# Kernel tuning notes

Measured on AMD Instinct MI355X. Metric: run time of the kernel, lower is better.

The kernel has to match this reference:

```python
import jax, jax.numpy as jnp
import numpy as np

B, L, M = 8192, 64, 64
LOCAL_DIM, MAX_UP, MAX_DN = 4, 64, 64


def setup_inputs() -> dict:
    key = jax.random.key(0)
    k1, k2 = jax.random.split(key)
    # occupation indices per site: 0=empty, 1=up, 2=down, 3=both
    indices = jax.random.randint(k1, (B, L), 0, LOCAL_DIM, dtype=jnp.int64)
    # learned GPS parameter tensor (local_dim, M, L, max_up+1, max_dn+1);
    # centered near 1 so the product over L sites stays numerically stable
    epsilon = 1.0 + 0.05 * jax.random.normal(
        k2, (LOCAL_DIM, M, L, MAX_UP + 1, MAX_DN + 1), dtype=jnp.float32)
    return {"indices": indices, "epsilon": epsilon}


def reference(indices, epsilon):
    b, l = indices.shape
    # cumulative particle counts of sites strictly before site i
    n_up = jnp.pad(jnp.cumsum(indices[:, :-1] & 1, axis=-1), ((0, 0), (1, 0)))
    n_dn = jnp.pad(jnp.cumsum((indices[:, :-1] & 2) // 2, axis=-1), ((0, 0), (1, 0)))
    site_ar = jnp.arange(l)[None, :]  # (1, L)
    # multi-axis gather: site_vals[b, i, m] = epsilon[idx[b,i], m, i, n_up[b,i], n_dn[b,i]]
    site_vals = epsilon[indices, :, site_ar, n_up, n_dn]  # (B, L, M)
    # product over sites, sum over GPS rank M
    log_psi = jnp.sum(jnp.prod(site_vals, axis=1), axis=-1)  # (B,)
    return log_psi
```

## Files before the change

kernel.cpp:

```cpp
#include <hip/hip_runtime.h>
#include <hip/hip_fp16.h>


#define TAB_HALF_BYTES ((size_t)89440 * 256 * 2)

__global__ __launch_bounds__(256) void seggps_init(int* __restrict__ ranges) {
  int t = threadIdx.x;
  if (t < 64) {
    ranges[t] = 64;
    ranges[64 + t] = -1;
    ranges[128 + t] = 64;
    ranges[192 + t] = -1;
  }
}

__global__ __launch_bounds__(256) void seggps_ranges(
    const int* __restrict__ indices, int* __restrict__ ranges) {
  __shared__ int s_umin[64], s_umax[64], s_nmin[64], s_nmax[64];
  int t = threadIdx.x;
  if (t < 64) { s_umin[t] = 64; s_umax[t] = -1; s_nmin[t] = 64; s_nmax[t] = -1; }
  __syncthreads();
  int wave = t >> 6, lane = t & 63;
  for (int i = 0; i < 16; ++i) {
    int b = blockIdx.x * 64 + wave * 16 + i;
    int v = indices[b * 64 + lane];
    int up = v & 1, dn = (v >> 1) & 1;
#pragma unroll
    for (int s = 1; s < 64; s <<= 1) {
      int au = __shfl_up(up, s, 64);
      int ad = __shfl_up(dn, s, 64);
      if (lane >= s) { up += au; dn += ad; }
    }
    int eu = up - (v & 1);
    int ed = dn - ((v >> 1) & 1);
    atomicMin(&s_umin[lane], eu); atomicMax(&s_umax[lane], eu);
    atomicMin(&s_nmin[lane], ed); atomicMax(&s_nmax[lane], ed);
  }
  __syncthreads();
  if (t < 64) {
    atomicMin(&ranges[t], s_umin[t]);
    atomicMax(&ranges[64 + t], s_umax[t]);
    atomicMin(&ranges[128 + t], s_nmin[t]);
    atomicMax(&ranges[192 + t], s_nmax[t]);
  }
}

__global__ __launch_bounds__(256) void seggps_transpose(
    const float* __restrict__ eps, __half* __restrict__ tab,
    const int* __restrict__ ranges) {
  int bid = blockIdx.x;
  int d = bid / 2080;
  int t = bid % 2080;
  int l = (int)((sqrtf(8.0f * (float)t + 1.0f) - 1.0f) * 0.5f);
  while ((l + 1) * (l + 2) / 2 <= t) ++l;
  while (l * (l + 1) / 2 > t) --l;
  int u = t - l * (l + 1) / 2;

  int umin = ranges[l], umax = ranges[64 + l];
  if (u < umin || u > umax) return;
  int nmin = ranges[128 + l], nmax = ranges[192 + l];

  int lane = threadIdx.x & 63;
  int wave = threadIdx.x >> 6;

  __shared__ float tile[64][65];

  const float* src = eps + ((size_t)(d * 64) * 64 + l) * 4225 + u * 65;
  if (lane >= nmin && lane <= nmax) {
#pragma unroll 4
    for (int m = wave; m < 64; m += 4) {
      tile[m][lane] = __builtin_nontemporal_load(&src[(size_t)m * 270400 + lane]);
    }
  }
  __syncthreads();

  int Pl = l * (l + 1) * (2 * l + 1) / 6;
  __half* dst = tab + (size_t)(Pl + u * (l + 1)) * 256 + d * 64 + lane;
  for (int n = nmin + wave; n <= nmax; n += 4) {
    dst[n * 256] = __float2half(tile[lane][n]);
  }
}

__global__ __launch_bounds__(256, 4) void seggps_main(
    const int* __restrict__ indices, const __half* __restrict__ tab,
    float* __restrict__ out) {
  int wave = threadIdx.x >> 6;
  int lane = threadIdx.x & 63;
  int g = lane >> 4;
  int Lm = lane & 15;
  int b0 = (blockIdx.x * 4 + wave) * 4;

  int ipk = indices[(b0 + 0) * 64 + lane]
          | (indices[(b0 + 1) * 64 + lane] << 2)
          | (indices[(b0 + 2) * 64 + lane] << 4)
          | (indices[(b0 + 3) * 64 + lane] << 6);

  float p0 = 1.f, p1 = 1.f, p2 = 1.f, p3 = 1.f;
  int up = 0, dn = 0;
  int Pl = 0;
  int mbase = Lm * 4;
#pragma unroll 16
  for (int l = 0; l < 64; ++l) {
    int s = __shfl(ipk, l, 64);
    int v = (s >> (2 * g)) & 3;
    int o = (Pl + up * (l + 1) + dn) * 256 + v * 64 + mbase;
    ushort4 q = *reinterpret_cast<const ushort4*>(tab + o);
    p0 *= __half2float(__ushort_as_half(q.x));
    p1 *= __half2float(__ushort_as_half(q.y));
    p2 *= __half2float(__ushort_as_half(q.z));
    p3 *= __half2float(__ushort_as_half(q.w));
    up += v & 1;
    dn += (v >> 1) & 1;
    Pl += (l + 1) * (l + 1);
  }
  float r = (p0 + p1) + (p2 + p3);
#pragma unroll
  for (int s = 8; s; s >>= 1) r += __shfl_down(r, s, 16);
  if (Lm == 0) out[b0 + g] = r;
}

__global__ __launch_bounds__(256) void seggps_direct(
    const int* __restrict__ indices, const float* __restrict__ eps,
    float* __restrict__ out) {
  int wave = threadIdx.x >> 6;
  int lane = threadIdx.x & 63;
  int b = blockIdx.x * 4 + wave;

  int myidx = indices[b * 64 + lane];

  float p0 = 1.f, p1 = 1.f, p2 = 1.f, p3 = 1.f;
  int up = 0, dn = 0;
#pragma unroll 8
  for (int l = 0; l < 64; ++l) {
    int v = __shfl(myidx, l, 64);
    size_t off = ((size_t)((v * 64 + lane) * 64 + l)) * 4225 + up * 65 + dn;
    float e = eps[off];
    if ((l & 3) == 0)      p0 *= e;
    else if ((l & 3) == 1) p1 *= e;
    else if ((l & 3) == 2) p2 *= e;
    else                   p3 *= e;
    up += v & 1;
    dn += (v >> 1) & 1;
  }
  float p = (p0 * p1) * (p2 * p3);
#pragma unroll
  for (int s = 32; s; s >>= 1) p += __shfl_down(p, s, 64);
  if (lane == 0) out[b] = p;
}

extern "C" void kernel_launch(void* const* d_in, const int* in_sizes, int n_in,
                              void* d_out, int out_size, void* d_ws, size_t ws_size,
                              hipStream_t stream) {
  const int* indices = (const int*)d_in[0];
  const float* eps   = (const float*)d_in[1];
  float* out = (float*)d_out;

  if (ws_size >= TAB_HALF_BYTES + 1024) {
    __half* tab = (__half*)d_ws;
    int* ranges = (int*)((char*)d_ws + TAB_HALF_BYTES);
    hipLaunchKernelGGL(seggps_init, dim3(1), dim3(256), 0, stream, ranges);
    hipLaunchKernelGGL(seggps_ranges, dim3(128), dim3(256), 0, stream,
                       indices, ranges);
    hipLaunchKernelGGL(seggps_transpose, dim3(4 * 2080), dim3(256), 0, stream,
                       eps, tab, ranges);
    hipLaunchKernelGGL(seggps_main, dim3(8192 / 16), dim3(256), 0, stream,
                       indices, tab, out);
  } else {
    hipLaunchKernelGGL(seggps_direct, dim3(8192 / 4), dim3(256), 0, stream,
                       indices, eps, out);
  }
}
```

Before: 341.8 us.

## Fuse four-kernel pipeline into one cooperative kernel with grid syncs

Replaces the init, ranges, transpose and main launches with a single cooperative kernel of 512 blocks that separates the phases with grid-wide syncs. The goal is to remove per-launch overhead and the tail gaps between kernels. The prefix count is now computed with ballot plus popcount instead of a shuffle scan, and the nontemporal load hint is dropped. In exchange, the transpose phase now runs on only 512 persistent blocks looping over 8320 items instead of 8320 independent blocks, which can cut memory-level parallelism. The grid barriers also add their own cost.

Result: slower. 500.5 us (+46.4%).

```diff
diff --git a/kernel.cpp b/kernel.cpp
--- a/kernel.cpp
+++ b/kernel.cpp
@@ -1,8 +1,120 @@
 #include <hip/hip_runtime.h>
 #include <hip/hip_fp16.h>
+#include <hip/hip_cooperative_groups.h>
+
+namespace cg = cooperative_groups;
 
 
 #define TAB_HALF_BYTES ((size_t)89440 * 256 * 2)
+
+__global__ __launch_bounds__(256, 2) void seggps_fused(
+    const int* __restrict__ indices, const float* __restrict__ eps,
+    __half* __restrict__ tab, int* __restrict__ ranges,
+    float* __restrict__ out) {
+  cg::grid_group grid = cg::this_grid();
+  __shared__ float tile[64][65];
+  __shared__ int s_umin[64], s_umax[64], s_nmin[64], s_nmax[64];
+
+  int t = threadIdx.x;
+  int wave = t >> 6, lane = t & 63;
+  int blk = blockIdx.x;
+
+  if (blk == 0 && t < 64) {
+    ranges[t] = 64;
+    ranges[64 + t] = -1;
+    ranges[128 + t] = 64;
+    ranges[192 + t] = -1;
+  }
+  if (t < 64) { s_umin[t] = 64; s_umax[t] = -1; s_nmin[t] = 64; s_nmax[t] = -1; }
+  grid.sync();
+
+  {
+    unsigned long long ltmask =
+        (lane == 63) ? 0x7fffffffffffffffull : ((1ull << lane) - 1ull);
+    for (int i = 0; i < 4; ++i) {
+      int b = blk * 16 + wave * 4 + i;
+      int v = indices[b * 64 + lane];
+      unsigned long long m0 = __ballot(v & 1);
+      unsigned long long m1 = __ballot(v & 2);
+      int eu = __popcll(m0 & ltmask);
+      int ed = __popcll(m1 & ltmask);
+      atomicMin(&s_umin[lane], eu); atomicMax(&s_umax[lane], eu);
+      atomicMin(&s_nmin[lane], ed); atomicMax(&s_nmax[lane], ed);
+    }
+    __syncthreads();
+    if (t < 64) {
+      atomicMin(&ranges[t], s_umin[t]);
+      atomicMax(&ranges[64 + t], s_umax[t]);
+      atomicMin(&ranges[128 + t], s_nmin[t]);
+      atomicMax(&ranges[192 + t], s_nmax[t]);
+    }
+  }
+  grid.sync();
+
+  for (int item = blk; item < 4 * 2080; item += 512) {
+    int d = item / 2080;
+    int tt = item % 2080;
+    int l = (int)((sqrtf(8.0f * (float)tt + 1.0f) - 1.0f) * 0.5f);
+    while ((l + 1) * (l + 2) / 2 <= tt) ++l;
+    while (l * (l + 1) / 2 > tt) --l;
+    int u = tt - l * (l + 1) / 2;
+
+    int umin = ranges[l], umax = ranges[64 + l];
+    if (u < umin || u > umax) continue;
+    int nmin = ranges[128 + l], nmax = ranges[192 + l];
+
+    const float* src = eps + ((size_t)(d * 64) * 64 + l) * 4225 + u * 65;
+    if (lane >= nmin && lane <= nmax) {
+#pragma unroll 4
+      for (int m = wave; m < 64; m += 4) {
+        tile[m][lane] = src[(size_t)m * 270400 + lane];
+      }
+    }
+    __syncthreads();
+
+    int Pl = l * (l + 1) * (2 * l + 1) / 6;
+    __half* dst = tab + (size_t)(Pl + u * (l + 1)) * 256 + d * 64 + lane;
+    for (int n = nmin + wave; n <= nmax; n += 4) {
+      dst[n * 256] = __float2half(tile[lane][n]);
+    }
+    __syncthreads();
+  }
+  grid.sync();
+
+  {
+    int g = lane >> 4;
+    int Lm = lane & 15;
+    int b0 = (blk * 4 + wave) * 4;
+
+    int ipk = indices[(b0 + 0) * 64 + lane]
+            | (indices[(b0 + 1) * 64 + lane] << 2)
+            | (indices[(b0 + 2) * 64 + lane] << 4)
+            | (indices[(b0 + 3) * 64 + lane] << 6);
+
+    float p0 = 1.f, p1 = 1.f, p2 = 1.f, p3 = 1.f;
+    int up = 0, dn = 0;
+    int Pl = 0;
+    int mbase = Lm * 4;
+#pragma unroll 16
+    for (int l = 0; l < 64; ++l) {
+      int s = __shfl(ipk, l, 64);
+      int v = (s >> (2 * g)) & 3;
+      int o = (Pl + up * (l + 1) + dn) * 256 + v * 64 + mbase;
+      ushort4 q = *reinterpret_cast<const ushort4*>(tab + o);
+      p0 *= __half2float(__ushort_as_half(q.x));
+      p1 *= __half2float(__ushort_as_half(q.y));
+      p2 *= __half2float(__ushort_as_half(q.z));
+      p3 *= __half2float(__ushort_as_half(q.w));
+      up += v & 1;
+      dn += (v >> 1) & 1;
+      Pl += (l + 1) * (l + 1);
+    }
+    float r = (p0 + p1) + (p2 + p3);
+#pragma unroll
+    for (int s2 = 8; s2; s2 >>= 1) r += __shfl_down(r, s2, 16);
+    if (Lm == 0) out[b0 + g] = r;
+  }
+}
 
 __global__ __launch_bounds__(256) void seggps_init(int* __restrict__ ranges) {
   int t = threadIdx.x;
@@ -21,18 +133,15 @@
   if (t < 64) { s_umin[t] = 64; s_umax[t] = -1; s_nmin[t] = 64; s_nmax[t] = -1; }
   __syncthreads();
   int wave = t >> 6, lane = t & 63;
+  unsigned long long ltmask =
+      (lane == 63) ? 0x7fffffffffffffffull : ((1ull << lane) - 1ull);
   for (int i = 0; i < 16; ++i) {
     int b = blockIdx.x * 64 + wave * 16 + i;
     int v = indices[b * 64 + lane];
-    int up = v & 1, dn = (v >> 1) & 1;
-#pragma unroll
-    for (int s = 1; s < 64; s <<= 1) {
-      int au = __shfl_up(up, s, 64);
-      int ad = __shfl_up(dn, s, 64);
-      if (lane >= s) { up += au; dn += ad; }
-    }
-    int eu = up - (v & 1);
-    int ed = dn - ((v >> 1) & 1);
+    unsigned long long m0 = __ballot(v & 1);
+    unsigned long long m1 = __ballot(v & 2);
+    int eu = __popcll(m0 & ltmask);
+    int ed = __popcll(m1 & ltmask);
     atomicMin(&s_umin[lane], eu); atomicMax(&s_umax[lane], eu);
     atomicMin(&s_nmin[lane], ed); atomicMax(&s_nmax[lane], ed);
   }
@@ -50,11 +159,11 @@
     const int* __restrict__ ranges) {
   int bid = blockIdx.x;
   int d = bid / 2080;
-  int t = bid % 2080;
-  int l = (int)((sqrtf(8.0f * (float)t + 1.0f) - 1.0f) * 0.5f);
-  while ((l + 1) * (l + 2) / 2 <= t) ++l;
-  while (l * (l + 1) / 2 > t) --l;
-  int u = t - l * (l + 1) / 2;
+  int tt = bid % 2080;
+  int l = (int)((sqrtf(8.0f * (float)tt + 1.0f) - 1.0f) * 0.5f);
+  while ((l + 1) * (l + 2) / 2 <= tt) ++l;
+  while (l * (l + 1) / 2 > tt) --l;
+  int u = tt - l * (l + 1) / 2;
 
   int umin = ranges[l], umax = ranges[64 + l];
   if (u < umin || u > umax) return;
@@ -69,7 +178,7 @@
   if (lane >= nmin && lane <= nmax) {
 #pragma unroll 4
     for (int m = wave; m < 64; m += 4) {
-      tile[m][lane] = __builtin_nontemporal_load(&src[(size_t)m * 270400 + lane]);
+      tile[m][lane] = src[(size_t)m * 270400 + lane];
     }
   }
   __syncthreads();
@@ -115,7 +224,7 @@
   }
   float r = (p0 + p1) + (p2 + p3);
 #pragma unroll
-  for (int s = 8; s; s >>= 1) r += __shfl_down(r, s, 16);
+  for (int s2 = 8; s2; s2 >>= 1) r += __shfl_down(r, s2, 16);
   if (Lm == 0) out[b0 + g] = r;
 }
 
@@ -158,13 +267,21 @@
   if (ws_size >= TAB_HALF_BYTES + 1024) {
     __half* tab = (__half*)d_ws;
     int* ranges = (int*)((char*)d_ws + TAB_HALF_BYTES);
-    hipLaunchKernelGGL(seggps_init, dim3(1), dim3(256), 0, stream, ranges);
-    hipLaunchKernelGGL(seggps_ranges, dim3(128), dim3(256), 0, stream,
-                       indices, ranges);
-    hipLaunchKernelGGL(seggps_transpose, dim3(4 * 2080), dim3(256), 0, stream,
-                       eps, tab, ranges);
-    hipLaunchKernelGGL(seggps_main, dim3(8192 / 16), dim3(256), 0, stream,
-                       indices, tab, out);
+
+    void* args[] = {(void*)&indices, (void*)&eps, (void*)&tab,
+                    (void*)&ranges, (void*)&out};
+    hipError_t e = hipLaunchCooperativeKernel(
+        (const void*)seggps_fused, dim3(512), dim3(256), args, 0, stream);
+    if (e != hipSuccess) {
+      (void)hipGetLastError();
+      hipLaunchKernelGGL(seggps_init, dim3(1), dim3(256), 0, stream, ranges);
+      hipLaunchKernelGGL(seggps_ranges, dim3(128), dim3(256), 0, stream,
+                         indices, ranges);
+      hipLaunchKernelGGL(seggps_transpose, dim3(4 * 2080), dim3(256), 0, stream,
+                         eps, tab, ranges);
+      hipLaunchKernelGGL(seggps_main, dim3(8192 / 16), dim3(256), 0, stream,
+                         indices, tab, out);
+    }
   } else {
     hipLaunchKernelGGL(seggps_direct, dim3(8192 / 4), dim3(256), 0, stream,
                        indices, eps, out);
```
